# Optimization experiments

Hardware: AMD Instinct MI355X
Metric: run time of the kernel (lower is better)

## Reference

```python
import math
import jax, jax.numpy as jnp
import numpy as np

HOP = 256
N_FFT = 1024
SR = 24000
B = 8
T = 1200          # feature frames
L = T * HOP       # 307200 audio samples
K_REV = 8192
BINS = N_FFT // 2 + 1


def setup_inputs() -> dict:
    key = jax.random.key(0)
    k1, k2, k3, k4, k5 = jax.random.split(key, 5)
    # realistic voiced f0 in [50, 400] Hz (forward gates on f0 > 20 Hz)
    f0 = 50.0 + 350.0 * jax.random.uniform(k1, (B, T), dtype=jnp.float32)
    env_per = jax.random.uniform(k2, (B, BINS, T), dtype=jnp.float32)
    env_noi = 0.1 * jax.random.uniform(k3, (B, BINS, T), dtype=jnp.float32)
    rev = 0.01 * jax.random.normal(k4, (B, K_REV), dtype=jnp.float32)
    # stands in for torch.rand_like(imp) inside forward (uniform [0,1))
    noi = jax.random.uniform(k5, (B, L), dtype=jnp.float32)
    # periodic Hann window, as torch.hann_window(n_fft)
    window = (0.5 - 0.5 * jnp.cos(2.0 * jnp.pi * jnp.arange(N_FFT) / N_FFT)).astype(jnp.float32)
    return {"f0": f0, "env_per": env_per, "env_noi": env_noi, "rev": rev, "noi": noi, "window": window}


def _interp_linear(x, scale):
    # torch F.interpolate(mode='linear', align_corners=False)
    Lx = x.shape[-1]
    out_len = Lx * scale
    src = (jnp.arange(out_len, dtype=jnp.float32) + 0.5) / scale - 0.5
    src = jnp.clip(src, 0.0, Lx - 1)
    i0 = jnp.floor(src).astype(jnp.int32)
    i1 = jnp.minimum(i0 + 1, Lx - 1)
    w = src - i0.astype(jnp.float32)
    return x[:, i0] * (1.0 - w) + x[:, i1] * w


def _stft(x, window):
    # torch.stft(center=True, pad_mode='reflect', return_complex=True)
    pad = N_FFT // 2
    xp = jnp.pad(x, ((0, 0), (pad, pad)), mode='reflect')
    n_frames = 1 + (xp.shape[-1] - N_FFT) // HOP
    idx = jnp.arange(n_frames)[:, None] * HOP + jnp.arange(N_FFT)[None, :]
    frames = xp[:, idx] * window                      # [B, F, N_FFT]
    return jnp.fft.rfft(frames, axis=-1).transpose(0, 2, 1)  # [B, BINS, F]


def _istft(spec, window):
    # torch.istft(center=True): windowed overlap-add with window-square normalization
    frames = jnp.fft.irfft(spec.transpose(0, 2, 1), n=N_FFT, axis=-1) * window  # [B, F, N_FFT]
    Bc, Fr, _ = frames.shape
    out_len = N_FFT + HOP * (Fr - 1)
    idx = (jnp.arange(Fr)[:, None] * HOP + jnp.arange(N_FFT)[None, :]).reshape(-1)
    out = jnp.zeros((Bc, out_len), frames.dtype).at[:, idx].add(frames.reshape(Bc, -1))
    wsq = jnp.zeros((out_len,), frames.dtype).at[idx].add(jnp.tile(window ** 2, Fr))
    out = out / jnp.where(wsq > 1e-11, wsq, 1.0)
    pad = N_FFT // 2
    return out[:, pad:out_len - pad]


def _min_phase(amp, eps=1e-5):
    # homomorphic minimum-phase reconstruction from real amplitude envelope
    # amp: [B, BINS, F]  ->  complex spectrum exp(rfft(lifted real cepstrum))
    log_amp = jnp.log(jnp.maximum(amp, eps))
    cep = jnp.fft.irfft(log_amp, n=N_FFT, axis=1)     # [B, N_FFT, F] real cepstrum
    lift = jnp.concatenate([
        jnp.ones((1,), jnp.float32),
        2.0 * jnp.ones((N_FFT // 2 - 1,), jnp.float32),
        jnp.ones((1,), jnp.float32),
        jnp.zeros((N_FFT // 2 - 1,), jnp.float32),
    ])
    return jnp.exp(jnp.fft.rfft(cep * lift[None, :, None], axis=1))  # [B, BINS, F]


def _fft_convolve(signal, kernel):
    # DDSP-style FFT convolution: zero-pad signal right, kernel left, multiply spectra
    Ls = signal.shape[-1]
    sig = jnp.pad(signal, ((0, 0), (0, Ls)))
    ker = jnp.pad(kernel, ((0, 0), (2 * Ls - kernel.shape[-1], 0)))
    out = jnp.fft.irfft(jnp.fft.rfft(sig) * jnp.fft.rfft(ker), n=2 * Ls)
    return out[:, Ls:]


def reference(f0, env_per, env_noi, rev, noi, window):
    env_per = jnp.pad(env_per, ((0, 0), (0, 0), (1, 0)))   # [B, BINS, T+1]
    env_noi = jnp.pad(env_noi, ((0, 0), (0, 0), (1, 0)))
    # sample-rate f0 track and impulse amplitude scale
    f0_up = _interp_linear(f0, HOP)                        # [B, L]
    imp_scale = jax.lax.rsqrt(jnp.maximum(f0_up, 20.0)) * math.sqrt(SR)
    # impulse train: fire where the running phase wraps past an integer
    phase = jnp.cumsum(f0_up, axis=-1) / SR
    saw = jnp.mod(phase, 1.0)
    imp = (saw - jnp.roll(saw, 1, axis=-1) < 0.0).astype(jnp.float32)
    imp = imp.at[:, 0].set(0.0)
    imp = imp * imp_scale
    imp_stft = _stft(imp, window)                          # [B, BINS, T+1]
    noi_stft = _stft(noi, window)
    # voiced/unvoiced gating of the periodic envelope
    mask = (jnp.pad(f0, ((0, 0), (1, 0)))[:, None, :] > 20.0).astype(jnp.float32)
    env_per = env_per * mask
    voi_stft = imp_stft * _min_phase(env_per) + noi_stft * env_noi
    voi = _istft(voi_stft, window)                         # [B, L]
    voi = _fft_convolve(voi, rev)                          # [B, L]
    return voi
```

## Files before the change

### kernel.cpp

```cpp
#include <hip/hip_runtime.h>
#include <math.h>

#define BB 8
#define TT 1200
#define NFFT 1024
#define BINS 513
#define LTOT 307200
#define KREV 8192
#define NFRM 34
#define NSAMP 8960
#define OUTOFF 299008
#define SQRT_SR 154.91933384829668f

#define OFF_FR   0

#define PHI(i) ((i) ^ ((i) >> 5))

__device__ __forceinline__ int rev4_10(int n) {
    int r = (int)(__brev((unsigned)n) >> 22);
    return ((r & 0x155) << 1) | ((r & 0x2AA) >> 1);
}

__device__ __forceinline__ void dif4(float* re, float* im,
                                     const float* twr, const float* twi,
                                     float dir, int u, bool act) {
#pragma unroll
    for (int s = 0; s < 5; ++s) {
        const int q = 256 >> (2 * s);
        const int sh = 8 - 2 * s;
        if (s < 2) __syncthreads();
        else       asm volatile("s_waitcnt lgkmcnt(0)" ::: "memory");
        if (act) {
            int t = u & (q - 1);
            int base = ((u >> sh) << (sh + 2)) | t;
            int i0 = PHI(base), i1 = PHI(base + q), i2 = PHI(base + 2 * q), i3 = PHI(base + 3 * q);
            float ar = re[i0], ai = im[i0];
            float br = re[i1], bi = im[i1];
            float cr = re[i2], ci = im[i2];
            float dr = re[i3], di = im[i3];
            float t0r = ar + cr, t0i = ai + ci;
            float t1r = ar - cr, t1i = ai - ci;
            float t2r = br + dr, t2i = bi + di;
            float t3r = br - dr, t3i = bi - di;
            float y0r = t0r + t2r, y0i = t0i + t2i;
            float y2r = t0r - t2r, y2i = t0i - t2i;
            float y1r = t1r - dir * t3i, y1i = t1i + dir * t3r;
            float y3r = t1r + dir * t3i, y3i = t1i - dir * t3r;
            float c1 = twr[2 * q - 1 + t], s1 = twi[2 * q - 1 + t];
            float c2 = twr[q - 1 + t],     s2 = twi[q - 1 + t];
            float w1r = c1, w1i = dir * s1;
            float w2r = c2, w2i = dir * s2;
            float w3r = c1 * c2 - s1 * s2;
            float w3i = dir * (c1 * s2 + s1 * c2);
            re[i0] = y0r;                       im[i0] = y0i;
            re[i1] = y1r * w1r - y1i * w1i;     im[i1] = y1r * w1i + y1i * w1r;
            re[i2] = y2r * w2r - y2i * w2i;     im[i2] = y2r * w2i + y2i * w2r;
            re[i3] = y3r * w3r - y3i * w3i;     im[i3] = y3r * w3i + y3i * w3r;
        }
    }
    __syncthreads();
}

__device__ __forceinline__ void dit4(float* re, float* im,
                                     const float* twr, const float* twi,
                                     float dir, int u, bool act) {
#pragma unroll
    for (int s = 0; s < 5; ++s) {
        const int q = 1 << (2 * s);
        const int sh = 2 * s;
        if (s == 0 || s == 4) __syncthreads();
        else                  asm volatile("s_waitcnt lgkmcnt(0)" ::: "memory");
        if (act) {
            int t = u & (q - 1);
            int base = ((u >> sh) << (sh + 2)) | t;
            int i0 = PHI(base), i1 = PHI(base + q), i2 = PHI(base + 2 * q), i3 = PHI(base + 3 * q);
            float c1 = twr[2 * q - 1 + t], s1 = twi[2 * q - 1 + t];
            float c2 = twr[q - 1 + t],     s2 = twi[q - 1 + t];
            float w1r = c1, w1i = dir * s1;
            float w2r = c2, w2i = dir * s2;
            float w3r = c1 * c2 - s1 * s2;
            float w3i = dir * (c1 * s2 + s1 * c2);
            float ar = re[i0], ai = im[i0];
            float xr = re[i1], xi = im[i1];
            float yr = re[i2], yi = im[i2];
            float zr = re[i3], zi = im[i3];
            float br = xr * w1r - xi * w1i, bi = xr * w1i + xi * w1r;
            float cr = yr * w2r - yi * w2i, ci = yr * w2i + yi * w2r;
            float dr = zr * w3r - zi * w3i, di = zr * w3i + zi * w3r;
            float t0r = ar + cr, t0i = ai + ci;
            float t1r = ar - cr, t1i = ai - ci;
            float t2r = br + dr, t2i = bi + di;
            float t3r = br - dr, t3i = bi - di;
            re[i0] = t0r + t2r;            im[i0] = t0i + t2i;
            re[i2] = t0r - t2r;            im[i2] = t0i - t2i;
            re[i1] = t1r - dir * t3i;      im[i1] = t1i + dir * t3r;
            re[i3] = t1r + dir * t3i;      im[i3] = t1i - dir * t3r;
        }
    }
    __syncthreads();
}

#define LV1 0
#define LV2 4480
#define LV3 6720
#define LV4 7840
#define LV5 8400
#define LV6 8680
#define LV7 8820
#define LV8 8890
#define LV9 8925
#define LV10 8942
#define LV11 8950
#define LV12 8954
#define LV13 8956

__global__ __launch_bounds__(512) void kfrm(const float* __restrict__ f0,
                                            const float* __restrict__ env_per,
                                            const float* __restrict__ env_noi,
                                            const float* __restrict__ noi,
                                            const float* __restrict__ win,
                                            float* __restrict__ W,
                                            float* __restrict__ out) {
    const int bid = blockIdx.x;
    const int tid = threadIdx.x;
    const int b = bid / 17;
    const int fp = (bid - b * 17) * 2;
    const int fg = fp + 1;

    __shared__ __align__(16) float SMEM[17917];
    __shared__ float cw[1281], fw[1281];
    __shared__ float twr[1023], twi[1023];

    const int idxF = (fp > 0) ? (fp - 1) : 0;
    const int idxG = fg - 1;
    float pfEpF = 0.f, pfEpG = 0.f, pfEpF2 = 0.f, pfEpG2 = 0.f;
    {
        pfEpF = env_per[((size_t)(b * BINS + tid)) * TT + idxF];
        pfEpG = env_per[((size_t)(b * BINS + tid)) * TT + idxG];
        if (tid == 0) {
            pfEpF2 = env_per[((size_t)(b * BINS + 512)) * TT + idxF];
            pfEpG2 = env_per[((size_t)(b * BINS + 512)) * TT + idxG];
        }
    }
    const float pfF0F = f0[b * TT + idxF];
    const float pfF0G = f0[b * TT + idxG];
    int ktmp0 = rev4_10(tid);
    const int kk0 = (ktmp0 <= 512) ? ktmp0 : 1024 - ktmp0;
    int ktmp1 = rev4_10(tid + 512);
    const int kk1 = (ktmp1 <= 512) ? ktmp1 : 1024 - ktmp1;
    const float pfEnF0 = env_noi[((size_t)(b * BINS + kk0)) * TT + idxF];
    const float pfEnG0 = env_noi[((size_t)(b * BINS + kk0)) * TT + idxG];
    const float pfEnF1 = env_noi[((size_t)(b * BINS + kk1)) * TT + idxF];
    const float pfEnG1 = env_noi[((size_t)(b * BINS + kk1)) * TT + idxG];
    int iF0 = 256 * fp + tid - 512; if (iF0 < 0) iF0 = -iF0;
    const int iF1 = 256 * fp + tid;
    int iG0 = 256 * fg + tid - 512; if (iG0 < 0) iG0 = -iG0;
    const int iG1 = 256 * fg + tid;
    const float pfNoiF0 = noi[(size_t)b * LTOT + iF0];
    const float pfNoiF1 = noi[(size_t)b * LTOT + iF1];
    const float pfNoiG0 = noi[(size_t)b * LTOT + iG0];
    const float pfNoiG1 = noi[(size_t)b * LTOT + iG1];
    const float pfWin0 = win[tid];
    const float pfWin1 = win[tid + 512];

    {
        float4* out4 = (float4*)out;
        int g = bid * 512 + tid;
        for (int idx = g; idx < (BB * LTOT) / 4; idx += 136 * 512)
            out4[idx] = make_float4(0.f, 0.f, 0.f, 0.f);
    }
    for (int x = tid; x < 1023; x += 512) {
        int hb = 31 - __clz(x + 1);
        int half = 1 << hb;
        int t = (x + 1) - half;
        float a = 3.14159265358979323846f * ((float)t / (float)half);
        float sv, cv; sincosf(a, &sv, &cv);
        twr[x] = cv; twi[x] = sv;
    }

    float* F = SMEM;
    float* L = SMEM + 8960;
    for (int i = tid; i < NSAMP; i += 512) {
        float src = __fsub_rn(__fdiv_rn(__fadd_rn((float)i, 0.5f), 256.0f), 0.5f);
        src = fminf(fmaxf(src, 0.0f), (float)(TT - 1));
        int i0 = (int)floorf(src);
        int i1 = i0 + 1; if (i1 > TT - 1) i1 = TT - 1;
        float w = __fsub_rn(src, (float)i0);
        float a0 = __fmul_rn(f0[b * TT + i0], __fsub_rn(1.0f, w));
        float a1 = __fmul_rn(f0[b * TT + i1], w);
        F[i] = __fadd_rn(a0, a1);
    }
    __syncthreads();
    for (int j = tid; j < 2240; j += 512) {
        float a = __fadd_rn(F[4*j],     F[4*j + 1]);
        float c = __fadd_rn(F[4*j + 2], F[4*j + 3]);
        L[LV1 + 2*j] = a; L[LV1 + 2*j + 1] = c;
        L[LV2 + j] = __fadd_rn(a, c);
    }
    __syncthreads();
    for (int j = tid; j < 560; j += 512) {
        float a = __fadd_rn(L[LV2 + 4*j],     L[LV2 + 4*j + 1]);
        float c = __fadd_rn(L[LV2 + 4*j + 2], L[LV2 + 4*j + 3]);
        L[LV3 + 2*j] = a; L[LV3 + 2*j + 1] = c;
        L[LV4 + j] = __fadd_rn(a, c);
    }
    __syncthreads();
    if (tid < 140) {
        int j = tid;
        float a = __fadd_rn(L[LV4 + 4*j],     L[LV4 + 4*j + 1]);
        float c = __fadd_rn(L[LV4 + 4*j + 2], L[LV4 + 4*j + 3]);
        L[LV5 + 2*j] = a; L[LV5 + 2*j + 1] = c;
        L[LV6 + j] = __fadd_rn(a, c);
    }
    __syncthreads();
    if (tid < 35) {
        int j = tid;
        float a = __fadd_rn(L[LV6 + 4*j],     L[LV6 + 4*j + 1]);
        float c = __fadd_rn(L[LV6 + 4*j + 2], L[LV6 + 4*j + 3]);
        L[LV7 + 2*j] = a; L[LV7 + 2*j + 1] = c;
        L[LV8 + j] = __fadd_rn(a, c);
    }
    __syncthreads();
    if (tid < 9) {
        int j = tid;
        if (j < 8) {
            float a = __fadd_rn(L[LV8 + 4*j],     L[LV8 + 4*j + 1]);
            float c = __fadd_rn(L[LV8 + 4*j + 2], L[LV8 + 4*j + 3]);
            L[LV9 + 2*j] = a; L[LV9 + 2*j + 1] = c;
            L[LV10 + j] = __fadd_rn(a, c);
        } else {
            L[LV9 + 16] = __fadd_rn(L[LV8 + 32], L[LV8 + 33]);
        }
    }
    __syncthreads();
    if (tid == 0) {
        float a0 = __fadd_rn(L[LV10 + 0], L[LV10 + 1]);
        float a1 = __fadd_rn(L[LV10 + 2], L[LV10 + 3]);
        float a2 = __fadd_rn(L[LV10 + 4], L[LV10 + 5]);
        float a3 = __fadd_rn(L[LV10 + 6], L[LV10 + 7]);
        L[LV11 + 0] = a0; L[LV11 + 1] = a1; L[LV11 + 2] = a2; L[LV11 + 3] = a3;
        float b0 = __fadd_rn(a0, a1), b1 = __fadd_rn(a2, a3);
        L[LV12 + 0] = b0; L[LV12 + 1] = b1;
        L[LV13 + 0] = __fadd_rn(b0, b1);
    }
    __syncthreads();
    const int cbase = (fp >= 3) ? (256 * fp - 513) : 0;
    {
        const int offs[14] = {0, LV1, LV2, LV3, LV4, LV5, LV6, LV7, LV8, LV9, LV10, LV11, LV12, LV13};
        for (int w = tid; w < 1281; w += 512) {
            int p = cbase + w;
            if (p < NSAMP) {
                int n = p + 1;
                float acc = 0.f; int pos = 0; bool first = true;
#pragma unroll
                for (int k = 13; k >= 1; --k) {
                    if ((n >> k) & 1) {
                        float t = L[offs[k] + (pos >> k)];
                        acc = first ? t : __fadd_rn(acc, t);
                        first = false;
                        pos += (1 << k);
                    }
                }
                if (n & 1) {
                    float t = F[pos];
                    acc = first ? t : __fadd_rn(acc, t);
                }
                cw[w] = acc;
                fw[w] = F[p];
            }
        }
    }
    __syncthreads();

    float* wr_  = SMEM;
    float* wi_  = SMEM + 1024;
    float* zfr  = SMEM + 2048;
    float* zfi  = SMEM + 3072;
    float* zgr  = SMEM + 4096;
    float* zgi  = SMEM + 5120;
    float* mpfr = SMEM + 6144;
    float* mpfi = SMEM + 6660;
    float* mpgr = SMEM + 7176;
    float* mpgi = SMEM + 7692;
    const int u = tid & 255;
    const bool lo = (tid < 256);

    {
        const bool gF = (fp > 0) && (pfF0F > 20.0f);
        const bool gG = (pfF0G > 20.0f);
        mpfr[tid] = logf(fmaxf(gF ? pfEpF : 0.0f, 1e-5f));
        mpgr[tid] = logf(fmaxf(gG ? pfEpG : 0.0f, 1e-5f));
        if (tid == 0) {
            mpfr[512] = logf(fmaxf(gF ? pfEpF2 : 0.0f, 1e-5f));
            mpgr[512] = logf(fmaxf(gG ? pfEpG2 : 0.0f, 1e-5f));
        }
    }
    __syncthreads();
#pragma unroll
    for (int r = 0; r < 2; ++r) {
        int n = tid + 512 * r;
        int kv = (n <= 512) ? n : 1024 - n;
        wr_[PHI(n)] = mpfr[kv];
        wi_[PHI(n)] = mpgr[kv];
    }
    dif4(wr_, wi_, twr, twi, -1.f, u, lo);
    const float inv = 1.0f / 1024.0f;
#pragma unroll
    for (int r = 0; r < 2; ++r) {
        int p = tid + 512 * r;
        int n = rev4_10(p);
        float wgt = (n == 0 || n == 512) ? inv : ((n < 512) ? 2.0f * inv : 0.0f);
        wr_[PHI(p)] *= wgt;
        wi_[PHI(p)] *= wgt;
    }
    dit4(wr_, wi_, twr, twi, -1.f, u, lo);
    for (int k = tid; k < BINS; k += 512) {
        int mk = (1024 - k) & 1023;
        float yr = wr_[PHI(k)], yi = wi_[PHI(k)];
        float ymr = wr_[PHI(mk)], ymi = -wi_[PHI(mk)];
        float Lfr = 0.5f * (yr + ymr), Lfi = 0.5f * (yi + ymi);
        float dr = yr - ymr, di = yi - ymi;
        float Lgr = 0.5f * di, Lgi = -0.5f * dr;
        float ef = expf(Lfr);
        mpfr[k] = ef * cosf(Lfi); mpfi[k] = ef * sinf(Lfi);
        float eg = expf(Lgr);
        mpgr[k] = eg * cosf(Lgi); mpgi[k] = eg * sinf(Lgi);
    }
    __syncthreads();
    {
        {
            const int n = tid;
            float v = 0.0f;
            int i = iF0;
            if (i > 0) {
                int iw = i - cbase;
                float ph  = __fdiv_rn(cw[iw], 24000.0f);
                float sw  = __fsub_rn(ph, floorf(ph));
                float ph2 = __fdiv_rn(cw[iw - 1], 24000.0f);
                float sw2 = __fsub_rn(ph2, floorf(ph2));
                if (__fsub_rn(sw, sw2) < 0.0f)
                    v = __fmul_rn(__fdiv_rn(1.0f, __fsqrt_rn(fmaxf(fw[iw], 20.0f))), SQRT_SR);
            }
            zfr[PHI(n)] = __fmul_rn(pfNoiF0, pfWin0);
            zfi[PHI(n)] = __fmul_rn(v, pfWin0);
            float v2 = 0.0f;
            int i2 = iG0;
            if (i2 > 0) {
                int iw = i2 - cbase;
                float ph  = __fdiv_rn(cw[iw], 24000.0f);
                float sw  = __fsub_rn(ph, floorf(ph));
                float ph2 = __fdiv_rn(cw[iw - 1], 24000.0f);
                float sw2 = __fsub_rn(ph2, floorf(ph2));
                if (__fsub_rn(sw, sw2) < 0.0f)
                    v2 = __fmul_rn(__fdiv_rn(1.0f, __fsqrt_rn(fmaxf(fw[iw], 20.0f))), SQRT_SR);
            }
            zgr[PHI(n)] = __fmul_rn(pfNoiG0, pfWin0);
            zgi[PHI(n)] = __fmul_rn(v2, pfWin0);
        }
        {
            const int n = tid + 512;
            float v = 0.0f;
            int i = iF1;
            if (i > 0) {
                int iw = i - cbase;
                float ph  = __fdiv_rn(cw[iw], 24000.0f);
                float sw  = __fsub_rn(ph, floorf(ph));
                float ph2 = __fdiv_rn(cw[iw - 1], 24000.0f);
                float sw2 = __fsub_rn(ph2, floorf(ph2));
                if (__fsub_rn(sw, sw2) < 0.0f)
                    v = __fmul_rn(__fdiv_rn(1.0f, __fsqrt_rn(fmaxf(fw[iw], 20.0f))), SQRT_SR);
            }
            zfr[PHI(n)] = __fmul_rn(pfNoiF1, pfWin1);
            zfi[PHI(n)] = __fmul_rn(v, pfWin1);
            float v2 = 0.0f;
            int i2 = iG1;
            if (i2 > 0) {
                int iw = i2 - cbase;
                float ph  = __fdiv_rn(cw[iw], 24000.0f);
                float sw  = __fsub_rn(ph, floorf(ph));
                float ph2 = __fdiv_rn(cw[iw - 1], 24000.0f);
                float sw2 = __fsub_rn(ph2, floorf(ph2));
                if (__fsub_rn(sw, sw2) < 0.0f)
                    v2 = __fmul_rn(__fdiv_rn(1.0f, __fsqrt_rn(fmaxf(fw[iw], 20.0f))), SQRT_SR);
            }
            zgr[PHI(n)] = __fmul_rn(pfNoiG1, pfWin1);
            zgi[PHI(n)] = __fmul_rn(v2, pfWin1);
        }
    }
    dif4(lo ? zfr : zgr, lo ? zfi : zgi, twr, twi, -1.f, u, true);
    {
        auto vbuild = [&](int p, int kk, float enF, float enG) {
            int k = rev4_10(p);
            bool cj = (k > 512);
            int p1 = rev4_10(kk);
            int p2 = rev4_10((1024 - kk) & 1023);
            float vr, vi;
            {
                float z1r = zfr[PHI(p1)], z1i = zfi[PHI(p1)];
                float z2r = zfr[PHI(p2)], z2i = -zfi[PHI(p2)];
                float Nr = 0.5f * (z1r + z2r), Ni = 0.5f * (z1i + z2i);
                float dr = z1r - z2r, di = z1i - z2i;
                float Ir = 0.5f * di, Ii = -0.5f * dr;
                float mpr = mpfr[kk], mpi2 = mpfi[kk];
                vr = Ir * mpr - Ii * mpi2 + Nr * enF;
                vi = Ir * mpi2 + Ii * mpr + Ni * enF;
                if (cj) vi = -vi;
            }
            float vgr, vgi;
            {
                float z1r = zgr[PHI(p1)], z1i = zgi[PHI(p1)];
                float z2r = zgr[PHI(p2)], z2i = -zgi[PHI(p2)];
                float Nr = 0.5f * (z1r + z2r), Ni = 0.5f * (z1i + z2i);
                float dr = z1r - z2r, di = z1i - z2i;
                float Ir = 0.5f * di, Ii = -0.5f * dr;
                float mpr = mpgr[kk], mpi2 = mpgi[kk];
                vgr = Ir * mpr - Ii * mpi2 + Nr * enG;
                vgi = Ir * mpi2 + Ii * mpr + Ni * enG;
                if (cj) vgi = -vgi;
            }
            wr_[PHI(p)] = vr - vgi;
            wi_[PHI(p)] = vi + vgr;
        };
        vbuild(tid,       kk0, (fp == 0) ? 0.0f : pfEnF0, pfEnG0);
        vbuild(tid + 512, kk1, (fp == 0) ? 0.0f : pfEnF1, pfEnG1);
    }
    dit4(wr_, wi_, twr, twi, +1.f, u, lo);
    {
        W[OFF_FR + (((size_t)(b * NFRM + fp)) << 10) + tid]       = __fmul_rn(__fmul_rn(wr_[PHI(tid)], inv), pfWin0);
        W[OFF_FR + (((size_t)(b * NFRM + fg)) << 10) + tid]       = __fmul_rn(__fmul_rn(wi_[PHI(tid)], inv), pfWin0);
        W[OFF_FR + (((size_t)(b * NFRM + fp)) << 10) + tid + 512] = __fmul_rn(__fmul_rn(wr_[PHI(tid + 512)], inv), pfWin1);
        W[OFF_FR + (((size_t)(b * NFRM + fg)) << 10) + tid + 512] = __fmul_rn(__fmul_rn(wi_[PHI(tid + 512)], inv), pfWin1);
    }
}

__global__ __launch_bounds__(256) void k4(const float* __restrict__ rev,
                                          const float* __restrict__ win,
                                          const float* __restrict__ W,
                                          float* __restrict__ out) {
    const int tid = threadIdx.x;
    const int b = blockIdx.x / 72;
    int r = blockIdx.x - b * 72;
    int jt = 0, acc0 = 0;
    while (acc0 + 2 * (jt + 1) <= r) { acc0 += 2 * (jt + 1); ++jt; }
    const int mc = r - acc0;
    const int j0 = jt << 10, m0 = mc << 9;

    __shared__ __align__(16) float S[1536];
    __shared__ __align__(16) float Rv[512];
    for (int x = tid; x < 512; x += 256)
        Rv[x] = rev[b * KREV + m0 + x];
    const int base = j0 - m0 - 512;
    for (int x = tid; x < 1536; x += 256) {
        int j = base + x;
        float v = 0.f;
        if (j >= 0 && j < KREV) {
            int s = j + 512;
            int flo = (s >= 1023) ? ((s - 1023 + 255) >> 8) : 0;
            int fhi = s >> 8; if (fhi > NFRM - 1) fhi = NFRM - 1;
            float acc = 0.f, wsq = 0.f;
            for (int f = flo; f <= fhi; ++f) {
                int o = s - (f << 8);
                acc = __fadd_rn(acc, W[OFF_FR + (((size_t)(b * NFRM + f)) << 10) + o]);
                float wv = win[o];
                wsq = __fadd_rn(wsq, __fmul_rn(wv, wv));
            }
            float den = (wsq > 1e-11f) ? wsq : 1.0f;
            v = __fdiv_rn(acc, den);
        }
        S[x] = v;
    }
    __syncthreads();

    const float4* S4 = (const float4*)S;
    const float4* R4 = (const float4*)Rv;
    float y0 = 0.f, y1 = 0.f, y2 = 0.f, y3 = 0.f;
    const int qi = tid + 128;
    float4 Bv = S4[qi];
#pragma unroll 4
    for (int mq = 0; mq < 128; ++mq) {
        float4 A = S4[qi - 1 - mq];
        float4 r4 = R4[mq];
        y0 = fmaf(r4.x, Bv.x, y0); y0 = fmaf(r4.y, A.w,  y0); y0 = fmaf(r4.z, A.z,  y0); y0 = fmaf(r4.w, A.y,  y0);
        y1 = fmaf(r4.x, Bv.y, y1); y1 = fmaf(r4.y, Bv.x, y1); y1 = fmaf(r4.z, A.w,  y1); y1 = fmaf(r4.w, A.z,  y1);
        y2 = fmaf(r4.x, Bv.z, y2); y2 = fmaf(r4.y, Bv.y, y2); y2 = fmaf(r4.z, Bv.x, y2); y2 = fmaf(r4.w, A.w,  y2);
        y3 = fmaf(r4.x, Bv.w, y3); y3 = fmaf(r4.y, Bv.z, y3); y3 = fmaf(r4.z, Bv.y, y3); y3 = fmaf(r4.w, Bv.x, y3);
        Bv = A;
    }
    float* o = out + (size_t)b * LTOT + OUTOFF + j0 + 4 * tid;
    atomicAdd(o + 0, y0);
    atomicAdd(o + 1, y1);
    atomicAdd(o + 2, y2);
    atomicAdd(o + 3, y3);
}

extern "C" void kernel_launch(void* const* d_in, const int* in_sizes, int n_in,
                              void* d_out, int out_size, void* d_ws, size_t ws_size,
                              hipStream_t stream) {
    const float* f0      = (const float*)d_in[0];
    const float* env_per = (const float*)d_in[1];
    const float* env_noi = (const float*)d_in[2];
    const float* rev     = (const float*)d_in[3];
    const float* noi     = (const float*)d_in[4];
    const float* win     = (const float*)d_in[5];
    float* out = (float*)d_out;
    float* W   = (float*)d_ws;

    kfrm<<<dim3(136), dim3(512), 0, stream>>>(f0, env_per, env_noi, noi, win, W, out);
    k4<<<dim3(576),   dim3(256), 0, stream>>>(rev, win, W, out);
}
```

Measured before the change: 142.1 us.

## Hoist per-batch cumsum and twiddle setup into a separate prologue kernel

A new 8-block kernel computes the upsampled f0, its prefix-sum tree and the FFT twiddle table once per batch and writes them to workspace. Previously each of the 136 frame blocks redid this for its whole batch. The frame kernel now only loads the window slice it needs, which shrinks its shared-memory footprint. It also moves the output zeroing to the end and sets many loops to unroll 1 to cut register use. The cost is an extra kernel launch with only 8 blocks and a global round-trip for the intermediates.

```diff
diff --git a/kernel.cpp b/kernel.cpp
--- a/kernel.cpp
+++ b/kernel.cpp
@@ -13,6 +13,9 @@
 #define SQRT_SR 154.91933384829668f
 
 #define OFF_FR   0
+#define OFF_CW   278528
+#define OFF_FW   350208
+#define OFF_TW   421888
 
 #define PHI(i) ((i) ^ ((i) >> 5))
 
@@ -24,7 +27,7 @@
 __device__ __forceinline__ void dif4(float* re, float* im,
                                      const float* twr, const float* twi,
                                      float dir, int u, bool act) {
-#pragma unroll
+#pragma unroll 1
     for (int s = 0; s < 5; ++s) {
         const int q = 256 >> (2 * s);
         const int sh = 8 - 2 * s;
@@ -64,7 +67,7 @@
 __device__ __forceinline__ void dit4(float* re, float* im,
                                      const float* twr, const float* twi,
                                      float dir, int u, bool act) {
-#pragma unroll
+#pragma unroll 1
     for (int s = 0; s < 5; ++s) {
         const int q = 1 << (2 * s);
         const int sh = 2 * s;
@@ -114,6 +117,113 @@
 #define LV12 8954
 #define LV13 8956
 
+__global__ __launch_bounds__(1024) void k0(const float* __restrict__ f0,
+                                           float* __restrict__ W) {
+    const int b = blockIdx.x;
+    const int tid = threadIdx.x;
+    __shared__ float F[NSAMP];
+    __shared__ float L[8957];
+
+    if (b == 0 && tid < 1023) {
+        int x = tid;
+        int hb = 31 - __clz(x + 1);
+        int half = 1 << hb;
+        int t = (x + 1) - half;
+        float a = 3.14159265358979323846f * ((float)t / (float)half);
+        float sv, cv; sincosf(a, &sv, &cv);
+        W[OFF_TW + x] = cv;
+        W[OFF_TW + 1023 + x] = sv;
+    }
+
+    for (int i = tid; i < NSAMP; i += 1024) {
+        float src = __fsub_rn(__fdiv_rn(__fadd_rn((float)i, 0.5f), 256.0f), 0.5f);
+        src = fminf(fmaxf(src, 0.0f), (float)(TT - 1));
+        int i0 = (int)floorf(src);
+        int i1 = i0 + 1; if (i1 > TT - 1) i1 = TT - 1;
+        float w = __fsub_rn(src, (float)i0);
+        float a0 = __fmul_rn(f0[b * TT + i0], __fsub_rn(1.0f, w));
+        float a1 = __fmul_rn(f0[b * TT + i1], w);
+        F[i] = __fadd_rn(a0, a1);
+    }
+    __syncthreads();
+    for (int j = tid; j < 2240; j += 1024) {
+        float a = __fadd_rn(F[4*j],     F[4*j + 1]);
+        float c = __fadd_rn(F[4*j + 2], F[4*j + 3]);
+        L[LV1 + 2*j] = a; L[LV1 + 2*j + 1] = c;
+        L[LV2 + j] = __fadd_rn(a, c);
+    }
+    __syncthreads();
+    if (tid < 560) {
+        int j = tid;
+        float a = __fadd_rn(L[LV2 + 4*j],     L[LV2 + 4*j + 1]);
+        float c = __fadd_rn(L[LV2 + 4*j + 2], L[LV2 + 4*j + 3]);
+        L[LV3 + 2*j] = a; L[LV3 + 2*j + 1] = c;
+        L[LV4 + j] = __fadd_rn(a, c);
+    }
+    __syncthreads();
+    if (tid < 140) {
+        int j = tid;
+        float a = __fadd_rn(L[LV4 + 4*j],     L[LV4 + 4*j + 1]);
+        float c = __fadd_rn(L[LV4 + 4*j + 2], L[LV4 + 4*j + 3]);
+        L[LV5 + 2*j] = a; L[LV5 + 2*j + 1] = c;
+        L[LV6 + j] = __fadd_rn(a, c);
+    }
+    __syncthreads();
+    if (tid < 35) {
+        int j = tid;
+        float a = __fadd_rn(L[LV6 + 4*j],     L[LV6 + 4*j + 1]);
+        float c = __fadd_rn(L[LV6 + 4*j + 2], L[LV6 + 4*j + 3]);
+        L[LV7 + 2*j] = a; L[LV7 + 2*j + 1] = c;
+        L[LV8 + j] = __fadd_rn(a, c);
+    }
+    __syncthreads();
+    if (tid < 9) {
+        int j = tid;
+        if (j < 8) {
+            float a = __fadd_rn(L[LV8 + 4*j],     L[LV8 + 4*j + 1]);
+            float c = __fadd_rn(L[LV8 + 4*j + 2], L[LV8 + 4*j + 3]);
+            L[LV9 + 2*j] = a; L[LV9 + 2*j + 1] = c;
+            L[LV10 + j] = __fadd_rn(a, c);
+        } else {
+            L[LV9 + 16] = __fadd_rn(L[LV8 + 32], L[LV8 + 33]);
+        }
+    }
+    __syncthreads();
+    if (tid == 0) {
+        float a0 = __fadd_rn(L[LV10 + 0], L[LV10 + 1]);
+        float a1 = __fadd_rn(L[LV10 + 2], L[LV10 + 3]);
+        float a2 = __fadd_rn(L[LV10 + 4], L[LV10 + 5]);
+        float a3 = __fadd_rn(L[LV10 + 6], L[LV10 + 7]);
+        L[LV11 + 0] = a0; L[LV11 + 1] = a1; L[LV11 + 2] = a2; L[LV11 + 3] = a3;
+        float b0 = __fadd_rn(a0, a1), b1 = __fadd_rn(a2, a3);
+        L[LV12 + 0] = b0; L[LV12 + 1] = b1;
+        L[LV13 + 0] = __fadd_rn(b0, b1);
+    }
+    __syncthreads();
+    {
+        const int offs[14] = {0, LV1, LV2, LV3, LV4, LV5, LV6, LV7, LV8, LV9, LV10, LV11, LV12, LV13};
+        for (int p = tid; p < NSAMP; p += 1024) {
+            int n = p + 1;
+            float acc = 0.f; int pos = 0; bool first = true;
+#pragma unroll
+            for (int k = 13; k >= 1; --k) {
+                if ((n >> k) & 1) {
+                    float t = L[offs[k] + (pos >> k)];
+                    acc = first ? t : __fadd_rn(acc, t);
+                    first = false;
+                    pos += (1 << k);
+                }
+            }
+            if (n & 1) {
+                float t = F[pos];
+                acc = first ? t : __fadd_rn(acc, t);
+            }
+            W[OFF_CW + b * NSAMP + p] = acc;
+            W[OFF_FW + b * NSAMP + p] = F[p];
+        }
+    }
+}
+
 __global__ __launch_bounds__(512) void kfrm(const float* __restrict__ f0,
                                             const float* __restrict__ env_per,
                                             const float* __restrict__ env_noi,
@@ -127,7 +237,7 @@
     const int fp = (bid - b * 17) * 2;
     const int fg = fp + 1;
 
-    __shared__ __align__(16) float SMEM[17917];
+    __shared__ __align__(16) float SMEM[8208];
     __shared__ float cw[1281], fw[1281];
     __shared__ float twr[1023], twi[1023];
 
@@ -163,114 +273,18 @@
     const float pfWin0 = win[tid];
     const float pfWin1 = win[tid + 512];
 
-    {
-        float4* out4 = (float4*)out;
-        int g = bid * 512 + tid;
-        for (int idx = g; idx < (BB * LTOT) / 4; idx += 136 * 512)
-            out4[idx] = make_float4(0.f, 0.f, 0.f, 0.f);
-    }
     for (int x = tid; x < 1023; x += 512) {
-        int hb = 31 - __clz(x + 1);
-        int half = 1 << hb;
-        int t = (x + 1) - half;
-        float a = 3.14159265358979323846f * ((float)t / (float)half);
-        float sv, cv; sincosf(a, &sv, &cv);
-        twr[x] = cv; twi[x] = sv;
-    }
-
-    float* F = SMEM;
-    float* L = SMEM + 8960;
-    for (int i = tid; i < NSAMP; i += 512) {
-        float src = __fsub_rn(__fdiv_rn(__fadd_rn((float)i, 0.5f), 256.0f), 0.5f);
-        src = fminf(fmaxf(src, 0.0f), (float)(TT - 1));
-        int i0 = (int)floorf(src);
-        int i1 = i0 + 1; if (i1 > TT - 1) i1 = TT - 1;
-        float w = __fsub_rn(src, (float)i0);
-        float a0 = __fmul_rn(f0[b * TT + i0], __fsub_rn(1.0f, w));
-        float a1 = __fmul_rn(f0[b * TT + i1], w);
-        F[i] = __fadd_rn(a0, a1);
-    }
-    __syncthreads();
-    for (int j = tid; j < 2240; j += 512) {
-        float a = __fadd_rn(F[4*j],     F[4*j + 1]);
-        float c = __fadd_rn(F[4*j + 2], F[4*j + 3]);
-        L[LV1 + 2*j] = a; L[LV1 + 2*j + 1] = c;
-        L[LV2 + j] = __fadd_rn(a, c);
-    }
-    __syncthreads();
-    for (int j = tid; j < 560; j += 512) {
-        float a = __fadd_rn(L[LV2 + 4*j],     L[LV2 + 4*j + 1]);
-        float c = __fadd_rn(L[LV2 + 4*j + 2], L[LV2 + 4*j + 3]);
-        L[LV3 + 2*j] = a; L[LV3 + 2*j + 1] = c;
-        L[LV4 + j] = __fadd_rn(a, c);
-    }
-    __syncthreads();
-    if (tid < 140) {
-        int j = tid;
-        float a = __fadd_rn(L[LV4 + 4*j],     L[LV4 + 4*j + 1]);
-        float c = __fadd_rn(L[LV4 + 4*j + 2], L[LV4 + 4*j + 3]);
-        L[LV5 + 2*j] = a; L[LV5 + 2*j + 1] = c;
-        L[LV6 + j] = __fadd_rn(a, c);
-    }
-    __syncthreads();
-    if (tid < 35) {
-        int j = tid;
-        float a = __fadd_rn(L[LV6 + 4*j],     L[LV6 + 4*j + 1]);
-        float c = __fadd_rn(L[LV6 + 4*j + 2], L[LV6 + 4*j + 3]);
-        L[LV7 + 2*j] = a; L[LV7 + 2*j + 1] = c;
-        L[LV8 + j] = __fadd_rn(a, c);
-    }
-    __syncthreads();
-    if (tid < 9) {
-        int j = tid;
-        if (j < 8) {
-            float a = __fadd_rn(L[LV8 + 4*j],     L[LV8 + 4*j + 1]);
-            float c = __fadd_rn(L[LV8 + 4*j + 2], L[LV8 + 4*j + 3]);
-            L[LV9 + 2*j] = a; L[LV9 + 2*j + 1] = c;
-            L[LV10 + j] = __fadd_rn(a, c);
-        } else {
-            L[LV9 + 16] = __fadd_rn(L[LV8 + 32], L[LV8 + 33]);
-        }
-    }
-    __syncthreads();
-    if (tid == 0) {
-        float a0 = __fadd_rn(L[LV10 + 0], L[LV10 + 1]);
-        float a1 = __fadd_rn(L[LV10 + 2], L[LV10 + 3]);
-        float a2 = __fadd_rn(L[LV10 + 4], L[LV10 + 5]);
-        float a3 = __fadd_rn(L[LV10 + 6], L[LV10 + 7]);
-        L[LV11 + 0] = a0; L[LV11 + 1] = a1; L[LV11 + 2] = a2; L[LV11 + 3] = a3;
-        float b0 = __fadd_rn(a0, a1), b1 = __fadd_rn(a2, a3);
-        L[LV12 + 0] = b0; L[LV12 + 1] = b1;
-        L[LV13 + 0] = __fadd_rn(b0, b1);
-    }
-    __syncthreads();
+        twr[x] = W[OFF_TW + x];
+        twi[x] = W[OFF_TW + 1023 + x];
+    }
     const int cbase = (fp >= 3) ? (256 * fp - 513) : 0;
-    {
-        const int offs[14] = {0, LV1, LV2, LV3, LV4, LV5, LV6, LV7, LV8, LV9, LV10, LV11, LV12, LV13};
-        for (int w = tid; w < 1281; w += 512) {
-            int p = cbase + w;
-            if (p < NSAMP) {
-                int n = p + 1;
-                float acc = 0.f; int pos = 0; bool first = true;
-#pragma unroll
-                for (int k = 13; k >= 1; --k) {
-                    if ((n >> k) & 1) {
-                        float t = L[offs[k] + (pos >> k)];
-                        acc = first ? t : __fadd_rn(acc, t);
-                        first = false;
-                        pos += (1 << k);
-                    }
-                }
-                if (n & 1) {
-                    float t = F[pos];
-                    acc = first ? t : __fadd_rn(acc, t);
-                }
-                cw[w] = acc;
-                fw[w] = F[p];
-            }
-        }
-    }
-    __syncthreads();
+    for (int w = tid; w < 1281; w += 512) {
+        int p = cbase + w;
+        if (p < NSAMP) {
+            cw[w] = W[OFF_CW + b * NSAMP + p];
+            fw[w] = W[OFF_FW + b * NSAMP + p];
+        }
+    }
 
     float* wr_  = SMEM;
     float* wi_  = SMEM + 1024;
@@ -296,18 +310,18 @@
         }
     }
     __syncthreads();
-#pragma unroll
+#pragma unroll 1
     for (int r = 0; r < 2; ++r) {
-        int n = tid + 512 * r;
+        int n = tid + (r << 9);
         int kv = (n <= 512) ? n : 1024 - n;
         wr_[PHI(n)] = mpfr[kv];
         wi_[PHI(n)] = mpgr[kv];
     }
     dif4(wr_, wi_, twr, twi, -1.f, u, lo);
     const float inv = 1.0f / 1024.0f;
-#pragma unroll
+#pragma unroll 1
     for (int r = 0; r < 2; ++r) {
-        int p = tid + 512 * r;
+        int p = tid + (r << 9);
         int n = rev4_10(p);
         float wgt = (n == 0 || n == 512) ? inv : ((n < 512) ? 2.0f * inv : 0.0f);
         wr_[PHI(p)] *= wgt;
@@ -327,11 +341,15 @@
         mpgr[k] = eg * cosf(Lgi); mpgi[k] = eg * sinf(Lgi);
     }
     __syncthreads();
-    {
-        {
-            const int n = tid;
+#pragma unroll 1
+    for (int r = 0; r < 2; ++r) {
+        const int n = tid + (r << 9);
+        const float wv = r ? pfWin1 : pfWin0;
+#pragma unroll 1
+        for (int h = 0; h < 2; ++h) {
+            int i = h ? (r ? iG1 : iG0) : (r ? iF1 : iF0);
+            float nv = h ? (r ? pfNoiG1 : pfNoiG0) : (r ? pfNoiF1 : pfNoiF0);
             float v = 0.0f;
-            int i = iF0;
             if (i > 0) {
                 int iw = i - cbase;
                 float ph  = __fdiv_rn(cw[iw], 24000.0f);
@@ -341,95 +359,64 @@
                 if (__fsub_rn(sw, sw2) < 0.0f)
                     v = __fmul_rn(__fdiv_rn(1.0f, __fsqrt_rn(fmaxf(fw[iw], 20.0f))), SQRT_SR);
             }
-            zfr[PHI(n)] = __fmul_rn(pfNoiF0, pfWin0);
-            zfi[PHI(n)] = __fmul_rn(v, pfWin0);
-            float v2 = 0.0f;
-            int i2 = iG0;
-            if (i2 > 0) {
-                int iw = i2 - cbase;
-                float ph  = __fdiv_rn(cw[iw], 24000.0f);
-                float sw  = __fsub_rn(ph, floorf(ph));
-                float ph2 = __fdiv_rn(cw[iw - 1], 24000.0f);
-                float sw2 = __fsub_rn(ph2, floorf(ph2));
-                if (__fsub_rn(sw, sw2) < 0.0f)
-                    v2 = __fmul_rn(__fdiv_rn(1.0f, __fsqrt_rn(fmaxf(fw[iw], 20.0f))), SQRT_SR);
-            }
-            zgr[PHI(n)] = __fmul_rn(pfNoiG0, pfWin0);
-            zgi[PHI(n)] = __fmul_rn(v2, pfWin0);
-        }
+            float* zr = h ? zgr : zfr;
+            float* zi = h ? zgi : zfi;
+            zr[PHI(n)] = __fmul_rn(nv, wv);
+            zi[PHI(n)] = __fmul_rn(v, wv);
+        }
+    }
+    dif4(lo ? zfr : zgr, lo ? zfi : zgi, twr, twi, -1.f, u, true);
+#pragma unroll 1
+    for (int r = 0; r < 2; ++r) {
+        int p = tid + (r << 9);
+        int kk = r ? kk1 : kk0;
+        float enF = (fp == 0) ? 0.0f : (r ? pfEnF1 : pfEnF0);
+        float enG = r ? pfEnG1 : pfEnG0;
+        int k = rev4_10(p);
+        bool cj = (k > 512);
+        int p1 = rev4_10(kk);
+        int p2 = rev4_10((1024 - kk) & 1023);
+        float vr, vi;
         {
-            const int n = tid + 512;
-            float v = 0.0f;
-            int i = iF1;
-            if (i > 0) {
-                int iw = i - cbase;
-                float ph  = __fdiv_rn(cw[iw], 24000.0f);
-                float sw  = __fsub_rn(ph, floorf(ph));
-                float ph2 = __fdiv_rn(cw[iw - 1], 24000.0f);
-                float sw2 = __fsub_rn(ph2, floorf(ph2));
-                if (__fsub_rn(sw, sw2) < 0.0f)
-                    v = __fmul_rn(__fdiv_rn(1.0f, __fsqrt_rn(fmaxf(fw[iw], 20.0f))), SQRT_SR);
-            }
-            zfr[PHI(n)] = __fmul_rn(pfNoiF1, pfWin1);
-            zfi[PHI(n)] = __fmul_rn(v, pfWin1);
-            float v2 = 0.0f;
-            int i2 = iG1;
-            if (i2 > 0) {
-                int iw = i2 - cbase;
-                float ph  = __fdiv_rn(cw[iw], 24000.0f);
-                float sw  = __fsub_rn(ph, floorf(ph));
-                float ph2 = __fdiv_rn(cw[iw - 1], 24000.0f);
-                float sw2 = __fsub_rn(ph2, floorf(ph2));
-                if (__fsub_rn(sw, sw2) < 0.0f)
-                    v2 = __fmul_rn(__fdiv_rn(1.0f, __fsqrt_rn(fmaxf(fw[iw], 20.0f))), SQRT_SR);
-            }
-            zgr[PHI(n)] = __fmul_rn(pfNoiG1, pfWin1);
-            zgi[PHI(n)] = __fmul_rn(v2, pfWin1);
-        }
-    }
-    dif4(lo ? zfr : zgr, lo ? zfi : zgi, twr, twi, -1.f, u, true);
+            float z1r = zfr[PHI(p1)], z1i = zfi[PHI(p1)];
+            float z2r = zfr[PHI(p2)], z2i = -zfi[PHI(p2)];
+            float Nr = 0.5f * (z1r + z2r), Ni = 0.5f * (z1i + z2i);
+            float dr = z1r - z2r, di = z1i - z2i;
+            float Ir = 0.5f * di, Ii = -0.5f * dr;
+            float mpr = mpfr[kk], mpi2 = mpfi[kk];
+            vr = Ir * mpr - Ii * mpi2 + Nr * enF;
+            vi = Ir * mpi2 + Ii * mpr + Ni * enF;
+            if (cj) vi = -vi;
+        }
+        float vgr, vgi;
+        {
+            float z1r = zgr[PHI(p1)], z1i = zgi[PHI(p1)];
+            float z2r = zgr[PHI(p2)], z2i = -zgi[PHI(p2)];
+            float Nr = 0.5f * (z1r + z2r), Ni = 0.5f * (z1i + z2i);
+            float dr = z1r - z2r, di = z1i - z2i;
+            float Ir = 0.5f * di, Ii = -0.5f * dr;
+            float mpr = mpgr[kk], mpi2 = mpgi[kk];
+            vgr = Ir * mpr - Ii * mpi2 + Nr * enG;
+            vgi = Ir * mpi2 + Ii * mpr + Ni * enG;
+            if (cj) vgi = -vgi;
+        }
+        wr_[PHI(p)] = vr - vgi;
+        wi_[PHI(p)] = vi + vgr;
+    }
+    dit4(wr_, wi_, twr, twi, +1.f, u, lo);
+#pragma unroll 1
+    for (int r = 0; r < 2; ++r) {
+        int n = tid + (r << 9);
+        float wv = r ? pfWin1 : pfWin0;
+        W[OFF_FR + (((size_t)(b * NFRM + fp)) << 10) + n] = __fmul_rn(__fmul_rn(wr_[PHI(n)], inv), wv);
+        W[OFF_FR + (((size_t)(b * NFRM + fg)) << 10) + n] = __fmul_rn(__fmul_rn(wi_[PHI(n)], inv), wv);
+    }
+
     {
-        auto vbuild = [&](int p, int kk, float enF, float enG) {
-            int k = rev4_10(p);
-            bool cj = (k > 512);
-            int p1 = rev4_10(kk);
-            int p2 = rev4_10((1024 - kk) & 1023);
-            float vr, vi;
-            {
-                float z1r = zfr[PHI(p1)], z1i = zfi[PHI(p1)];
-                float z2r = zfr[PHI(p2)], z2i = -zfi[PHI(p2)];
-                float Nr = 0.5f * (z1r + z2r), Ni = 0.5f * (z1i + z2i);
-                float dr = z1r - z2r, di = z1i - z2i;
-                float Ir = 0.5f * di, Ii = -0.5f * dr;
-                float mpr = mpfr[kk], mpi2 = mpfi[kk];
-                vr = Ir * mpr - Ii * mpi2 + Nr * enF;
-                vi = Ir * mpi2 + Ii * mpr + Ni * enF;
-                if (cj) vi = -vi;
-            }
-            float vgr, vgi;
-            {
-                float z1r = zgr[PHI(p1)], z1i = zgi[PHI(p1)];
-                float z2r = zgr[PHI(p2)], z2i = -zgi[PHI(p2)];
-                float Nr = 0.5f * (z1r + z2r), Ni = 0.5f * (z1i + z2i);
-                float dr = z1r - z2r, di = z1i - z2i;
-                float Ir = 0.5f * di, Ii = -0.5f * dr;
-                float mpr = mpgr[kk], mpi2 = mpgi[kk];
-                vgr = Ir * mpr - Ii * mpi2 + Nr * enG;
-                vgi = Ir * mpi2 + Ii * mpr + Ni * enG;
-                if (cj) vgi = -vgi;
-            }
-            wr_[PHI(p)] = vr - vgi;
-            wi_[PHI(p)] = vi + vgr;
-        };
-        vbuild(tid,       kk0, (fp == 0) ? 0.0f : pfEnF0, pfEnG0);
-        vbuild(tid + 512, kk1, (fp == 0) ? 0.0f : pfEnF1, pfEnG1);
-    }
-    dit4(wr_, wi_, twr, twi, +1.f, u, lo);
-    {
-        W[OFF_FR + (((size_t)(b * NFRM + fp)) << 10) + tid]       = __fmul_rn(__fmul_rn(wr_[PHI(tid)], inv), pfWin0);
-        W[OFF_FR + (((size_t)(b * NFRM + fg)) << 10) + tid]       = __fmul_rn(__fmul_rn(wi_[PHI(tid)], inv), pfWin0);
-        W[OFF_FR + (((size_t)(b * NFRM + fp)) << 10) + tid + 512] = __fmul_rn(__fmul_rn(wr_[PHI(tid + 512)], inv), pfWin1);
-        W[OFF_FR + (((size_t)(b * NFRM + fg)) << 10) + tid + 512] = __fmul_rn(__fmul_rn(wi_[PHI(tid + 512)], inv), pfWin1);
+        float4* out4 = (float4*)out;
+        int g = bid * 512 + tid;
+        for (int idx = g; idx < (BB * LTOT) / 4; idx += 136 * 512)
+            out4[idx] = make_float4(0.f, 0.f, 0.f, 0.f);
     }
 }
 
@@ -505,6 +492,7 @@
     float* out = (float*)d_out;
     float* W   = (float*)d_ws;
 
-    kfrm<<<dim3(136), dim3(512), 0, stream>>>(f0, env_per, env_noi, noi, win, W, out);
-    k4<<<dim3(576),   dim3(256), 0, stream>>>(rev, win, W, out);
-}
+    k0<<<dim3(8),     dim3(1024), 0, stream>>>(f0, W);
+    kfrm<<<dim3(136), dim3(512),  0, stream>>>(f0, env_per, env_noi, noi, win, W, out);
+    k4<<<dim3(576),   dim3(256),  0, stream>>>(rev, win, W, out);
+}
```

Result: slower. 150.4 us (+5.8%).

## Use packed FP32 FMA with reversed swizzled LDS layout in reverb convolution

Applied to the files above, without the earlier changes.

The direct-convolution inner loop of k4 is rebuilt around v_pk_fma_f32. The signal tile is stored reversed in two LDS copies offset by one sample, with an XOR swizzle, so each thread reads aligned float2 pairs and computes outputs of one parity. This is meant to halve the FMA instruction count and cut LDS bank conflicts. The cost is double LDS storage, inline asm, and a changed summation order.

```diff
diff --git a/kernel.cpp b/kernel.cpp
--- a/kernel.cpp
+++ b/kernel.cpp
@@ -15,6 +15,10 @@
 #define OFF_FR   0
 
 #define PHI(i) ((i) ^ ((i) >> 5))
+
+typedef float f2 __attribute__((ext_vector_type(2)));
+
+#define PK(A, B, C) asm("v_pk_fma_f32 %0, %1, %2, %0" : "+v"(A) : "v"(B), "v"(C))
 
 __device__ __forceinline__ int rev4_10(int n) {
     int r = (int)(__brev((unsigned)n) >> 22);
@@ -433,6 +437,11 @@
     }
 }
 
+__device__ __forceinline__ f2 ldw(const float* A, int p) {
+    int ps = p ^ ((p >> 4) & 15);
+    return *(const f2*)(A + 2 * ps);
+}
+
 __global__ __launch_bounds__(256) void k4(const float* __restrict__ rev,
                                           const float* __restrict__ win,
                                           const float* __restrict__ W,
@@ -445,10 +454,13 @@
     const int mc = r - acc0;
     const int j0 = jt << 10, m0 = mc << 9;
 
-    __shared__ __align__(16) float S[1536];
-    __shared__ __align__(16) float Rv[512];
+    __shared__ __align__(16) float TaF[1536];
+    __shared__ __align__(16) float TbF[1536];
+    __shared__ __align__(16) float RvF[512];
+
     for (int x = tid; x < 512; x += 256)
-        Rv[x] = rev[b * KREV + m0 + x];
+        RvF[x] = rev[b * KREV + m0 + x];
+
     const int base = j0 - m0 - 512;
     for (int x = tid; x < 1536; x += 256) {
         int j = base + x;
@@ -467,30 +479,49 @@
             float den = (wsq > 1e-11f) ? wsq : 1.0f;
             v = __fdiv_rn(acc, den);
         }
-        S[x] = v;
-    }
-    __syncthreads();
-
-    const float4* S4 = (const float4*)S;
-    const float4* R4 = (const float4*)Rv;
-    float y0 = 0.f, y1 = 0.f, y2 = 0.f, y3 = 0.f;
-    const int qi = tid + 128;
-    float4 Bv = S4[qi];
-#pragma unroll 4
-    for (int mq = 0; mq < 128; ++mq) {
-        float4 A = S4[qi - 1 - mq];
-        float4 r4 = R4[mq];
-        y0 = fmaf(r4.x, Bv.x, y0); y0 = fmaf(r4.y, A.w,  y0); y0 = fmaf(r4.z, A.z,  y0); y0 = fmaf(r4.w, A.y,  y0);
-        y1 = fmaf(r4.x, Bv.y, y1); y1 = fmaf(r4.y, Bv.x, y1); y1 = fmaf(r4.z, A.w,  y1); y1 = fmaf(r4.w, A.z,  y1);
-        y2 = fmaf(r4.x, Bv.z, y2); y2 = fmaf(r4.y, Bv.y, y2); y2 = fmaf(r4.z, Bv.x, y2); y2 = fmaf(r4.w, A.w,  y2);
-        y3 = fmaf(r4.x, Bv.w, y3); y3 = fmaf(r4.y, Bv.z, y3); y3 = fmaf(r4.z, Bv.y, y3); y3 = fmaf(r4.w, Bv.x, y3);
-        Bv = A;
-    }
-    float* o = out + (size_t)b * LTOT + OUTOFF + j0 + 4 * tid;
-    atomicAdd(o + 0, y0);
-    atomicAdd(o + 1, y1);
-    atomicAdd(o + 2, y2);
-    atomicAdd(o + 3, y3);
+        int t = 1535 - x;
+        {
+            int pa = t >> 1, ea = t & 1;
+            int ps = pa ^ ((pa >> 4) & 15);
+            TaF[2 * ps + ea] = v;
+        }
+        int q = t - 1;
+        if (q >= 0) {
+            int pb = q >> 1, eb = q & 1;
+            int ps = pb ^ ((pb >> 4) & 15);
+            TbF[2 * ps + eb] = v;
+        }
+    }
+    __syncthreads();
+
+    const int par = tid & 1;
+    const int g = tid >> 1;
+    const float* Tx = par ? TaF : TbF;
+    const int B = 511 - 4 * g;
+    const f2* R2 = (const f2*)RvF;
+
+    f2 a0 = (f2){0.f, 0.f}, a1 = a0, a2 = a0, a3 = a0;
+    f2 w0 = ldw(Tx, B - 3);
+    f2 w1 = ldw(Tx, B - 2);
+    f2 w2 = ldw(Tx, B - 1);
+    f2 w3, rc;
+
+    for (int i0 = 0; i0 < 256; i0 += 4) {
+        w3 = ldw(Tx, B + i0);     rc = R2[i0];
+        PK(a0, rc, w3); PK(a1, rc, w2); PK(a2, rc, w1); PK(a3, rc, w0);
+        w0 = ldw(Tx, B + i0 + 1); rc = R2[i0 + 1];
+        PK(a0, rc, w0); PK(a1, rc, w3); PK(a2, rc, w2); PK(a3, rc, w1);
+        w1 = ldw(Tx, B + i0 + 2); rc = R2[i0 + 2];
+        PK(a0, rc, w1); PK(a1, rc, w0); PK(a2, rc, w3); PK(a3, rc, w2);
+        w2 = ldw(Tx, B + i0 + 3); rc = R2[i0 + 3];
+        PK(a0, rc, w2); PK(a1, rc, w1); PK(a2, rc, w0); PK(a3, rc, w3);
+    }
+
+    float* o = out + (size_t)b * LTOT + OUTOFF + j0 + 8 * g + par;
+    atomicAdd(o + 0, a0.x + a0.y);
+    atomicAdd(o + 2, a1.x + a1.y);
+    atomicAdd(o + 4, a2.x + a2.y);
+    atomicAdd(o + 6, a3.x + a3.y);
 }
 
 extern "C" void kernel_launch(void* const* d_in, const int* in_sizes, int n_in,
```

Result: faster. 134.5 us (-5.4%).
